# Kernel optimization log

Hardware: AMD Instinct MI355X
Metric: run time of the kernel (lower is better)

## Reference

```python
import jax, jax.numpy as jnp
import numpy as np

N = 100_000   # nodes
E = 1_600_000 # edges (avg degree 16)
B = 512       # graphs in batch
F_IN = 64; H = 4; D = 64; HD = H * D; EXTRA = 16
NEG_SLOPE = 0.2  # DGL GATConv default


def _gat_conv(x, src, dst, W, al, ar, bias):
    """DGL GATConv: fc -> per-head attn logits -> edge leaky_relu -> segment softmax over dst -> scatter-sum."""
    h = (x @ W).reshape(N, H, D)                       # [N,H,D]
    el = jnp.sum(h * al, axis=-1)                      # [N,H]
    er = jnp.sum(h * ar, axis=-1)                      # [N,H]
    e = jax.nn.leaky_relu(el[src] + er[dst], NEG_SLOPE)  # [E,H]
    m = jax.ops.segment_max(e, dst, num_segments=N)    # [N,H]
    m = jnp.where(jnp.isfinite(m), m, 0.0)             # guard empty segments
    ex = jnp.exp(e - m[dst])                           # [E,H]
    den = jax.ops.segment_sum(ex, dst, num_segments=N) # [N,H]
    alpha = ex / jnp.maximum(den[dst], 1e-9)           # [E,H]
    msg = h[src] * alpha[:, :, None]                   # [E,H,D]
    out = jax.ops.segment_sum(msg, dst, num_segments=N) + bias.reshape(1, H, D)
    return out  # [N,H,D]


def setup_inputs() -> dict:
    key = jax.random.key(0)
    ks = jax.random.split(key, 26)
    nrm = lambda k, shape: jax.random.normal(k, shape, dtype=jnp.float32) * 0.5
    src = jax.random.randint(ks[0], (E,), 0, N)
    # ensure every node has >=1 incoming edge (DGL disallows zero in-degree by default)
    dst = jnp.concatenate([jnp.arange(N), jax.random.randint(ks[1], (E - N,), 0, N)])
    node_graph = jnp.sort(jax.random.randint(ks[2], (N,), 0, B))
    inp = dict(
        src=src, dst=dst, node_graph=node_graph,
        feats_node=jax.random.normal(ks[3], (N, F_IN), dtype=jnp.float32),
        feats_graph=jax.random.normal(ks[4], (B, EXTRA), dtype=jnp.float32),
        W1=nrm(ks[5], (F_IN, HD)), al1=nrm(ks[6], (H, D)), ar1=nrm(ks[7], (H, D)), bg1=jnp.zeros(HD),
        W2=nrm(ks[8], (HD, HD)),  al2=nrm(ks[9], (H, D)), ar2=nrm(ks[10], (H, D)), bg2=jnp.zeros(HD),
        W3=nrm(ks[11], (HD, HD)), al3=nrm(ks[12], (H, D)), ar3=nrm(ks[13], (H, D)), bg3=jnp.zeros(HD),
        sw=nrm(ks[14], (HD, 1)), sb=jnp.zeros(1),
        lw1=nrm(ks[15], (HD + EXTRA, 2 * D)), lb1=jnp.zeros(2 * D),
        lw2=nrm(ks[16], (2 * D, D)), lb2=jnp.zeros(D),
        lw3=nrm(ks[17], (D, 1)), lb3=jnp.zeros(1),
    )
    return inp


def reference(src, dst, node_graph, feats_node, feats_graph,
              W1, al1, ar1, bg1, W2, al2, ar2, bg2, W3, al3, ar3, bg3,
              sw, sb, lw1, lb1, lw2, lb2, lw3, lb3):
    selu = jax.nn.selu
    x = selu(_gat_conv(feats_node, src, dst, W1, al1, ar1, bg1)).reshape(N, HD)
    x = selu(_gat_conv(x, src, dst, W2, al2, ar2, bg2)).reshape(N, HD)
    x = selu(_gat_conv(x, src, dst, W3, al3, ar3, bg3)).reshape(N, HD)
    # WeightedAverage readout: sigmoid-scored weighted mean per graph
    w = jax.nn.sigmoid(x @ sw + sb)                               # [N,1]
    num = jax.ops.segment_sum(w * x, node_graph, num_segments=B)  # [B,HD]
    den = jax.ops.segment_sum(w, node_graph, num_segments=B)      # [B,1]
    emb = num / jnp.maximum(den, 1e-9)
    y = jnp.concatenate([emb, feats_graph], axis=1)
    y = selu(y @ lw1 + lb1)
    y = selu(y @ lw2 + lb2)
    return y @ lw3 + lb3  # [B,1]
```

## Files before the change

kernel.cpp:

```cpp
#include <hip/hip_runtime.h>

#define N_NODES 100000
#define N_EDGES 1600000
#define N_GRAPHS 512
#define F_IN 64
#define HD 256
#define EXTRA 16
#define SCAN_BLOCK 512

typedef float f32x4 __attribute__((ext_vector_type(4)));
typedef _Float16 f16x4 __attribute__((ext_vector_type(4)));
typedef _Float16 f16x8 __attribute__((ext_vector_type(8)));

__device__ __forceinline__ float selu_f(float x) {
    const float a = 1.6732632423543772f, sc = 1.0507009873554805f;
    return x > 0.f ? sc * x : sc * a * (__expf(x) - 1.f);
}

__global__ __launch_bounds__(256) void hist_k(const int* __restrict__ dst, int* __restrict__ hist) {
    int j = blockIdx.x * 256 + threadIdx.x;
    if (j < N_EDGES) atomicAdd(&hist[dst[j]], 1);
}

__global__ __launch_bounds__(SCAN_BLOCK) void scan1_k(const int* __restrict__ hist,
                                                      int* __restrict__ row_ptr,
                                                      int* __restrict__ bsums) {
    __shared__ int sm[SCAN_BLOCK];
    int t = threadIdx.x;
    int i = blockIdx.x * SCAN_BLOCK + t;
    int v = (i < N_NODES) ? hist[i] : 0;
    sm[t] = v;
    __syncthreads();
    for (int off = 1; off < SCAN_BLOCK; off <<= 1) {
        int add = (t >= off) ? sm[t - off] : 0;
        __syncthreads();
        sm[t] += add;
        __syncthreads();
    }
    if (i < N_NODES) row_ptr[i] = sm[t] - v;
    if (t == SCAN_BLOCK - 1) bsums[blockIdx.x] = sm[t];
}

__global__ __launch_bounds__(256) void scan2_k(int* __restrict__ bsums, int nb) {
    __shared__ int sm[256];
    int t = threadIdx.x;
    int v = (t < nb) ? bsums[t] : 0;
    sm[t] = v;
    __syncthreads();
    for (int off = 1; off < 256; off <<= 1) {
        int add = (t >= off) ? sm[t - off] : 0;
        __syncthreads();
        sm[t] += add;
        __syncthreads();
    }
    if (t < nb) bsums[t] = sm[t] - v;
}

__global__ __launch_bounds__(256) void scan3_k(int* __restrict__ row_ptr, const int* __restrict__ bsums) {
    int i = blockIdx.x * 256 + threadIdx.x;
    if (i < N_NODES) row_ptr[i] += bsums[i / SCAN_BLOCK];
    if (i == 0) row_ptr[N_NODES] = N_EDGES;
}

__global__ __launch_bounds__(256) void scatter_k(const int* __restrict__ src,
                                                 const int* __restrict__ dst,
                                                 const int* __restrict__ row_ptr,
                                                 int* __restrict__ cursor,
                                                 int* __restrict__ csr_src) {
    int j = blockIdx.x * 256 + threadIdx.x;
    if (j < N_EDGES) {
        int d = dst[j];
        int r = atomicAdd(&cursor[d], 1);
        csr_src[row_ptr[d] + r] = src[j];
    }
}

__global__ __launch_bounds__(256) void gbound_k(const int* __restrict__ node_graph, int* __restrict__ gstart) {
    int g = blockIdx.x * 256 + threadIdx.x;
    if (g > N_GRAPHS) return;
    int lo = 0, hi = N_NODES;
    while (lo < hi) {
        int mid = (lo + hi) >> 1;
        if (node_graph[mid] < g) lo = mid + 1; else hi = mid;
    }
    gstart[g] = lo;
}

__global__ __launch_bounds__(256) void tcast_split_k(const float* __restrict__ W,
                                                     _Float16* __restrict__ Wt_hi,
                                                     _Float16* __restrict__ Wt_lo, int K) {
    int idx = blockIdx.x * 256 + threadIdx.x;
    if (idx >= K * HD) return;
    int n = idx / K, k = idx - n * K;
    float w = W[(size_t)k * HD + n];
    _Float16 hi = (_Float16)w;
    _Float16 lo = (_Float16)(w - (float)hi);
    Wt_hi[idx] = hi;
    Wt_lo[idx] = lo;
}

template <int K>
__global__ __launch_bounds__(256) void gemm_split_k(const float* __restrict__ A,
                                                    const _Float16* __restrict__ Bt_hi,
                                                    const _Float16* __restrict__ Bt_lo,
                                                    const float* __restrict__ al,
                                                    const float* __restrict__ ar,
                                                    _Float16* __restrict__ Chi,
                                                    float* __restrict__ el,
                                                    float* __restrict__ er, int M) {
    const int BM = 128, BN = 128, LDP = 40;
    __shared__ _Float16 As_hi[BM][LDP];
    __shared__ _Float16 As_lo[BM][LDP];
    __shared__ _Float16 Bs_hi[BN][LDP];
    __shared__ _Float16 Bs_lo[BN][LDP];
    int tid = threadIdx.x;
    int wave = tid >> 6, lane = tid & 63;
    int q = lane >> 4, l16 = lane & 15;
    int row0 = blockIdx.y * BM, col0 = blockIdx.x * BN;
    f32x4 acc[2][8] = {};

    for (int k0 = 0; k0 < K; k0 += 32) {
#pragma unroll
        for (int c = 0; c < 4; c++) {
            int cc = tid + c * 256;
            int r = cc >> 3, o = (cc & 7) * 4;
            int gr = row0 + r;
            float4 v = make_float4(0.f, 0.f, 0.f, 0.f);
            if (gr < M) v = *(const float4*)(A + (size_t)gr * K + k0 + o);
            f16x4 hi, lo;
            hi.x = (_Float16)v.x; lo.x = (_Float16)(v.x - (float)hi.x);
            hi.y = (_Float16)v.y; lo.y = (_Float16)(v.y - (float)hi.y);
            hi.z = (_Float16)v.z; lo.z = (_Float16)(v.z - (float)hi.z);
            hi.w = (_Float16)v.w; lo.w = (_Float16)(v.w - (float)hi.w);
            *(f16x4*)&As_hi[r][o] = hi;
            *(f16x4*)&As_lo[r][o] = lo;
        }
#pragma unroll
        for (int c = 0; c < 2; c++) {
            int cc = tid + c * 256;
            int n = cc >> 2, o = (cc & 3) * 8;
            *(f16x8*)&Bs_hi[n][o] = *(const f16x8*)(Bt_hi + (size_t)(col0 + n) * K + k0 + o);
            *(f16x8*)&Bs_lo[n][o] = *(const f16x8*)(Bt_lo + (size_t)(col0 + n) * K + k0 + o);
        }
        __syncthreads();

        f16x8 ah[2], alo2[2];
#pragma unroll
        for (int ms = 0; ms < 2; ms++) {
            int m = wave * 32 + ms * 16 + l16;
            ah[ms] = *(const f16x8*)&As_hi[m][q * 8];
            alo2[ms] = *(const f16x8*)&As_lo[m][q * 8];
        }
#pragma unroll
        for (int ns = 0; ns < 8; ns++) {
            int n = ns * 16 + l16;
            f16x8 bh = *(const f16x8*)&Bs_hi[n][q * 8];
            f16x8 bl = *(const f16x8*)&Bs_lo[n][q * 8];
#pragma unroll
            for (int ms = 0; ms < 2; ms++) {
                acc[ms][ns] = __builtin_amdgcn_mfma_f32_16x16x32_f16(ah[ms], bh, acc[ms][ns], 0, 0, 0);
                acc[ms][ns] = __builtin_amdgcn_mfma_f32_16x16x32_f16(ah[ms], bl, acc[ms][ns], 0, 0, 0);
                acc[ms][ns] = __builtin_amdgcn_mfma_f32_16x16x32_f16(alo2[ms], bh, acc[ms][ns], 0, 0, 0);
            }
        }
        __syncthreads();
    }

    const int h0 = col0 >> 6;
    float alv[8], arv[8];
#pragma unroll
    for (int ns = 0; ns < 8; ns++) {
        int hh = h0 + (ns >> 2);
        int d = (ns & 3) * 16 + l16;
        alv[ns] = al[hh * 64 + d];
        arv[ns] = ar[hh * 64 + d];
    }
#pragma unroll
    for (int ms = 0; ms < 2; ms++) {
#pragma unroll
        for (int i = 0; i < 4; i++) {
            int r = row0 + wave * 32 + ms * 16 + q * 4 + i;
            bool ok = r < M;
            float el0 = 0.f, er0 = 0.f, el1 = 0.f, er1 = 0.f;
#pragma unroll
            for (int ns = 0; ns < 8; ns++) {
                float v = acc[ms][ns][i];
                if (ok) Chi[(size_t)r * HD + col0 + ns * 16 + l16] = (_Float16)v;
                if (ns < 4) { el0 = fmaf(v, alv[ns], el0); er0 = fmaf(v, arv[ns], er0); }
                else        { el1 = fmaf(v, alv[ns], el1); er1 = fmaf(v, arv[ns], er1); }
            }
#pragma unroll
            for (int off = 1; off < 16; off <<= 1) {
                el0 += __shfl_xor(el0, off, 64);
                er0 += __shfl_xor(er0, off, 64);
                el1 += __shfl_xor(el1, off, 64);
                er1 += __shfl_xor(er1, off, 64);
            }
            if (l16 == 0 && ok) {
                el[(size_t)r * 4 + h0] = el0;
                el[(size_t)r * 4 + h0 + 1] = el1;
                er[(size_t)r * 4 + h0] = er0;
                er[(size_t)r * 4 + h0 + 1] = er1;
            }
        }
    }
}

template <int OUT>
__global__ __launch_bounds__(256) void gat_aggregate_k(const _Float16* __restrict__ hb,
                                                       const float* __restrict__ el,
                                                       const float* __restrict__ er,
                                                       const int* __restrict__ csr_src,
                                                       const int* __restrict__ row_ptr,
                                                       const float* __restrict__ bias,
                                                       float* __restrict__ xout,
                                                       const float* __restrict__ sw,
                                                       const float* __restrict__ sb,
                                                       float* __restrict__ wsc) {
    __shared__ float wlds[4][64][4];
    __shared__ int snlds[4][64];
    int wv = threadIdx.x >> 6;
    int lane = threadIdx.x & 63;
    int v = blockIdx.x * 4 + wv;
    bool valid = v < N_NODES;
    int vc = valid ? v : 0;
    int rs = row_ptr[vc];
    int deg = valid ? row_ptr[vc + 1] - rs : 0;
    float4 erv = make_float4(0.f, 0.f, 0.f, 0.f);
    if (valid) erv = *(const float4*)(er + (size_t)vc * 4);

    int head = lane >> 4;
    float inv_den = 1.f;
    float m_h = 0.f, er_h = 0.f;

    if (deg <= 64) {
        float e0 = -1e30f, e1 = -1e30f, e2 = -1e30f, e3 = -1e30f;
        int my_sn = 0;
        if (lane < deg) {
            my_sn = csr_src[rs + lane];
            float4 elv = *(const float4*)(el + (size_t)my_sn * 4);
            float t0 = elv.x + erv.x, t1 = elv.y + erv.y, t2 = elv.z + erv.z, t3 = elv.w + erv.w;
            e0 = t0 > 0.f ? t0 : 0.2f * t0;
            e1 = t1 > 0.f ? t1 : 0.2f * t1;
            e2 = t2 > 0.f ? t2 : 0.2f * t2;
            e3 = t3 > 0.f ? t3 : 0.2f * t3;
        }
        float m0 = e0, m1 = e1, m2 = e2, m3 = e3;
        for (int off = 1; off < deg; off <<= 1) {
            m0 = fmaxf(m0, __shfl_xor(m0, off, 64));
            m1 = fmaxf(m1, __shfl_xor(m1, off, 64));
            m2 = fmaxf(m2, __shfl_xor(m2, off, 64));
            m3 = fmaxf(m3, __shfl_xor(m3, off, 64));
        }
        float p0 = 0.f, p1 = 0.f, p2 = 0.f, p3 = 0.f;
        if (lane < deg) {
            p0 = __expf(e0 - m0); p1 = __expf(e1 - m1);
            p2 = __expf(e2 - m2); p3 = __expf(e3 - m3);
        }
        float s0 = p0, s1 = p1, s2 = p2, s3 = p3;
        for (int off = 1; off < deg; off <<= 1) {
            s0 += __shfl_xor(s0, off, 64);
            s1 += __shfl_xor(s1, off, 64);
            s2 += __shfl_xor(s2, off, 64);
            s3 += __shfl_xor(s3, off, 64);
        }
        float d0 = __shfl(s0, 0, 64), d1 = __shfl(s1, 0, 64);
        float d2 = __shfl(s2, 0, 64), d3 = __shfl(s3, 0, 64);
        float den = head == 0 ? d0 : head == 1 ? d1 : head == 2 ? d2 : d3;
        inv_den = 1.f / fmaxf(den, 1e-9f);
        if (lane < deg) {
            wlds[wv][lane][0] = p0;
            wlds[wv][lane][1] = p1;
            wlds[wv][lane][2] = p2;
            wlds[wv][lane][3] = p3;
            snlds[wv][lane] = my_sn;
        }
    } else {
        float m[4] = {-1e30f, -1e30f, -1e30f, -1e30f};
        float s[4] = {0.f, 0.f, 0.f, 0.f};
        for (int t = lane; t < deg; t += 64) {
            int sn = csr_src[rs + t];
            float4 elv = *(const float4*)(el + (size_t)sn * 4);
            float e[4];
            e[0] = elv.x + erv.x; e[1] = elv.y + erv.y; e[2] = elv.z + erv.z; e[3] = elv.w + erv.w;
#pragma unroll
            for (int hh = 0; hh < 4; hh++) {
                float ev = e[hh] > 0.f ? e[hh] : 0.2f * e[hh];
                float mn = fmaxf(m[hh], ev);
                s[hh] = s[hh] * __expf(m[hh] - mn) + __expf(ev - mn);
                m[hh] = mn;
            }
        }
#pragma unroll
        for (int off = 32; off >= 1; off >>= 1) {
#pragma unroll
            for (int hh = 0; hh < 4; hh++) {
                float mo = __shfl_xor(m[hh], off, 64);
                float so = __shfl_xor(s[hh], off, 64);
                float mn = fmaxf(m[hh], mo);
                s[hh] = s[hh] * __expf(m[hh] - mn) + so * __expf(mo - mn);
                m[hh] = mn;
            }
        }
        m_h = head == 0 ? m[0] : head == 1 ? m[1] : head == 2 ? m[2] : m[3];
        float den = head == 0 ? s[0] : head == 1 ? s[1] : head == 2 ? s[2] : s[3];
        er_h = head == 0 ? erv.x : head == 1 ? erv.y : head == 2 ? erv.z : erv.w;
        inv_den = 1.f / fmaxf(den, 1e-9f);
    }
    __syncthreads();

    float a0 = 0.f, a1 = 0.f, a2 = 0.f, a3 = 0.f;
    if (deg <= 64) {
        int t = 0;
        for (; t + 8 <= deg; t += 8) {
            int sn[8];
            float w[8];
#pragma unroll
            for (int u = 0; u < 8; u++) {
                sn[u] = snlds[wv][t + u];
                w[u] = wlds[wv][t + u][head];
            }
            f16x4 hv[8];
#pragma unroll
            for (int u = 0; u < 8; u++)
                hv[u] = *(const f16x4*)(hb + (size_t)sn[u] * HD + lane * 4);
#pragma unroll
            for (int u = 0; u < 8; u++) {
                a0 = fmaf(w[u], (float)hv[u].x, a0);
                a1 = fmaf(w[u], (float)hv[u].y, a1);
                a2 = fmaf(w[u], (float)hv[u].z, a2);
                a3 = fmaf(w[u], (float)hv[u].w, a3);
            }
        }
        for (; t < deg; t++) {
            int sn = snlds[wv][t];
            float w = wlds[wv][t][head];
            f16x4 hv = *(const f16x4*)(hb + (size_t)sn * HD + lane * 4);
            a0 = fmaf(w, (float)hv.x, a0);
            a1 = fmaf(w, (float)hv.y, a1);
            a2 = fmaf(w, (float)hv.z, a2);
            a3 = fmaf(w, (float)hv.w, a3);
        }
    } else {
        for (int t = 0; t < deg; t++) {
            int sn = csr_src[rs + t];
            float e = el[(size_t)sn * 4 + head] + er_h;
            e = e > 0.f ? e : 0.2f * e;
            float w = __expf(e - m_h);
            f16x4 hv = *(const f16x4*)(hb + (size_t)sn * HD + lane * 4);
            a0 = fmaf(w, (float)hv.x, a0);
            a1 = fmaf(w, (float)hv.y, a1);
            a2 = fmaf(w, (float)hv.z, a2);
            a3 = fmaf(w, (float)hv.w, a3);
        }
    }
    float4 bv = *(const float4*)(bias + lane * 4);
    float4 o;
    o.x = selu_f(fmaf(a0, inv_den, bv.x));
    o.y = selu_f(fmaf(a1, inv_den, bv.y));
    o.z = selu_f(fmaf(a2, inv_den, bv.z));
    o.w = selu_f(fmaf(a3, inv_den, bv.w));
    if (valid) *(float4*)(xout + (size_t)v * HD + lane * 4) = o;

    if constexpr (OUT == 1) {
        float4 sv = *(const float4*)(sw + lane * 4);
        float p = o.x * sv.x + o.y * sv.y + o.z * sv.z + o.w * sv.w;
#pragma unroll
        for (int off = 1; off < 64; off <<= 1) p += __shfl_xor(p, off, 64);
        if (lane == 0 && valid) wsc[v] = 1.f / (1.f + __expf(-(p + sb[0])));
    }
}

__global__ __launch_bounds__(256) void readout_k(const float* __restrict__ x,
                                                 const float* __restrict__ wsc,
                                                 const int* __restrict__ gstart,
                                                 const float* __restrict__ fg,
                                                 float* __restrict__ y0) {
    int g = blockIdx.x;
    int f = threadIdx.x;
    int s = gstart[g], e = gstart[g + 1];
    float num = 0.f, den = 0.f;
#pragma unroll 4
    for (int n = s; n < e; n++) {
        float wn = wsc[n];
        num = fmaf(wn, x[(size_t)n * HD + f], num);
        den += wn;
    }
    float emb = num / fmaxf(den, 1e-9f);
    y0[(size_t)g * 272 + f] = emb;
    if (f < EXTRA) y0[(size_t)g * 272 + 256 + f] = fg[g * EXTRA + f];
}

__global__ __launch_bounds__(128) void mlp_k(const float* __restrict__ y0g,
                                             const float* __restrict__ lw1, const float* __restrict__ lb1,
                                             const float* __restrict__ lw2, const float* __restrict__ lb2,
                                             const float* __restrict__ lw3, const float* __restrict__ lb3,
                                             float* __restrict__ out) {
    __shared__ float y0s[272];
    __shared__ float y1s[128];
    int g = blockIdx.x, t = threadIdx.x;
    for (int i = t; i < 272; i += 128) y0s[i] = y0g[(size_t)g * 272 + i];
    __syncthreads();
    float acc = lb1[t];
    for (int k = 0; k < 272; k++) acc = fmaf(y0s[k], lw1[k * 128 + t], acc);
    y1s[t] = selu_f(acc);
    __syncthreads();
    if (t < 64) {
        float a2 = lb2[t];
        for (int k = 0; k < 128; k++) a2 = fmaf(y1s[k], lw2[k * 64 + t], a2);
        float v2 = selu_f(a2);
        float p = v2 * lw3[t];
#pragma unroll
        for (int off = 1; off < 64; off <<= 1) p += __shfl_xor(p, off, 64);
        if (t == 0) out[g] = p + lb3[0];
    }
}

extern "C" void kernel_launch(void* const* d_in, const int* in_sizes, int n_in,
                              void* d_out, int out_size, void* d_ws, size_t ws_size,
                              hipStream_t stream) {
    const int* src = (const int*)d_in[0];
    const int* dst = (const int*)d_in[1];
    const int* node_graph = (const int*)d_in[2];
    const float* feats_node = (const float*)d_in[3];
    const float* feats_graph = (const float*)d_in[4];
    const float* W1 = (const float*)d_in[5];
    const float* al1 = (const float*)d_in[6];
    const float* ar1 = (const float*)d_in[7];
    const float* bg1 = (const float*)d_in[8];
    const float* W2 = (const float*)d_in[9];
    const float* al2 = (const float*)d_in[10];
    const float* ar2 = (const float*)d_in[11];
    const float* bg2 = (const float*)d_in[12];
    const float* W3 = (const float*)d_in[13];
    const float* al3 = (const float*)d_in[14];
    const float* ar3 = (const float*)d_in[15];
    const float* bg3 = (const float*)d_in[16];
    const float* sw = (const float*)d_in[17];
    const float* sb = (const float*)d_in[18];
    const float* lw1 = (const float*)d_in[19];
    const float* lb1 = (const float*)d_in[20];
    const float* lw2 = (const float*)d_in[21];
    const float* lb2 = (const float*)d_in[22];
    const float* lw3 = (const float*)d_in[23];
    const float* lb3 = (const float*)d_in[24];
    float* out = (float*)d_out;

    char* ws = (char*)d_ws;
    size_t off = 0;
    auto alloc = [&](size_t bytes) -> char* {
        char* p = ws + off;
        off += (bytes + 255) & ~(size_t)255;
        return p;
    };
    float* xf32 = (float*)alloc((size_t)N_NODES * HD * 4);
    _Float16* hhi = (_Float16*)alloc((size_t)N_NODES * HD * 2);
    _Float16* W1hi = (_Float16*)alloc((size_t)F_IN * HD * 2);
    _Float16* W1lo = (_Float16*)alloc((size_t)F_IN * HD * 2);
    _Float16* W2hi = (_Float16*)alloc((size_t)HD * HD * 2);
    _Float16* W2lo = (_Float16*)alloc((size_t)HD * HD * 2);
    _Float16* W3hi = (_Float16*)alloc((size_t)HD * HD * 2);
    _Float16* W3lo = (_Float16*)alloc((size_t)HD * HD * 2);
    float* el = (float*)alloc((size_t)N_NODES * 4 * 4);
    float* er = (float*)alloc((size_t)N_NODES * 4 * 4);
    float* wsc = (float*)alloc((size_t)N_NODES * 4);
    float* y0 = (float*)alloc((size_t)N_GRAPHS * 272 * 4);
    int* hist = (int*)alloc((size_t)N_NODES * 4);
    int* row_ptr = (int*)alloc((size_t)(N_NODES + 1) * 4);
    int* cursor = (int*)alloc((size_t)N_NODES * 4);
    int* csr_src = (int*)alloc((size_t)N_EDGES * 4);
    int* gstart = (int*)alloc((size_t)(N_GRAPHS + 1) * 4);
    int* bsums = (int*)alloc(256 * 4);
    (void)ws_size; (void)in_sizes; (void)n_in; (void)out_size;

    hipMemsetAsync(hist, 0, (size_t)N_NODES * 4, stream);
    hipMemsetAsync(cursor, 0, (size_t)N_NODES * 4, stream);

    hist_k<<<(N_EDGES + 255) / 256, 256, 0, stream>>>(dst, hist);
    int nb = (N_NODES + SCAN_BLOCK - 1) / SCAN_BLOCK;
    scan1_k<<<nb, SCAN_BLOCK, 0, stream>>>(hist, row_ptr, bsums);
    scan2_k<<<1, 256, 0, stream>>>(bsums, nb);
    scan3_k<<<(N_NODES + 255) / 256, 256, 0, stream>>>(row_ptr, bsums);
    scatter_k<<<(N_EDGES + 255) / 256, 256, 0, stream>>>(src, dst, row_ptr, cursor, csr_src);
    gbound_k<<<3, 256, 0, stream>>>(node_graph, gstart);

    tcast_split_k<<<(F_IN * HD + 255) / 256, 256, 0, stream>>>(W1, W1hi, W1lo, F_IN);
    tcast_split_k<<<(HD * HD + 255) / 256, 256, 0, stream>>>(W2, W2hi, W2lo, HD);
    tcast_split_k<<<(HD * HD + 255) / 256, 256, 0, stream>>>(W3, W3hi, W3lo, HD);

    dim3 ggrid(HD / 128, (N_NODES + 127) / 128);
    int nwb = (N_NODES + 3) / 4;

    gemm_split_k<F_IN><<<ggrid, 256, 0, stream>>>(feats_node, W1hi, W1lo, al1, ar1, hhi, el, er, N_NODES);
    gat_aggregate_k<0><<<nwb, 256, 0, stream>>>(hhi, el, er, csr_src, row_ptr, bg1, xf32, nullptr, nullptr, nullptr);
    gemm_split_k<HD><<<ggrid, 256, 0, stream>>>(xf32, W2hi, W2lo, al2, ar2, hhi, el, er, N_NODES);
    gat_aggregate_k<0><<<nwb, 256, 0, stream>>>(hhi, el, er, csr_src, row_ptr, bg2, xf32, nullptr, nullptr, nullptr);
    gemm_split_k<HD><<<ggrid, 256, 0, stream>>>(xf32, W3hi, W3lo, al3, ar3, hhi, el, er, N_NODES);
    gat_aggregate_k<1><<<nwb, 256, 0, stream>>>(hhi, el, er, csr_src, row_ptr, bg3, xf32, sw, sb, wsc);

    readout_k<<<N_GRAPHS, 256, 0, stream>>>(xf32, wsc, gstart, feats_graph, y0);
    mlp_k<<<N_GRAPHS, 128, 0, stream>>>(y0, lw1, lb1, lw2, lb2, lw3, lb3, out);
}
```

Before: 973.0 us.

## Store activations as fp16 hi/lo split, prefetch neighbors, simplify CSR scatter

The aggregate kernel now writes layer outputs directly as fp16 hi/lo pairs, so the following GEMM loads pre-split halves instead of fp32 values and converting in its tile loader. Input features get a separate split-cast kernel. The aggregation prefetches the first eight neighbor rows before the softmax reductions and drops a __syncthreads. The CSR scatter seeds its cursor with row_ptr, which removes a memset and an extra row_ptr read per edge. The split representation moves the same number of bytes as fp32, and the xf32 buffer now aliases xhi.

```diff
diff --git a/kernel.cpp b/kernel.cpp
--- a/kernel.cpp
+++ b/kernel.cpp
@@ -56,22 +56,25 @@
     if (t < nb) bsums[t] = sm[t] - v;
 }
 
-__global__ __launch_bounds__(256) void scan3_k(int* __restrict__ row_ptr, const int* __restrict__ bsums) {
+__global__ __launch_bounds__(256) void scan3_k(int* __restrict__ row_ptr, const int* __restrict__ bsums,
+                                               int* __restrict__ cursor) {
     int i = blockIdx.x * 256 + threadIdx.x;
-    if (i < N_NODES) row_ptr[i] += bsums[i / SCAN_BLOCK];
+    if (i < N_NODES) {
+        int r = row_ptr[i] + bsums[i / SCAN_BLOCK];
+        row_ptr[i] = r;
+        cursor[i] = r;
+    }
     if (i == 0) row_ptr[N_NODES] = N_EDGES;
 }
 
 __global__ __launch_bounds__(256) void scatter_k(const int* __restrict__ src,
                                                  const int* __restrict__ dst,
-                                                 const int* __restrict__ row_ptr,
                                                  int* __restrict__ cursor,
                                                  int* __restrict__ csr_src) {
     int j = blockIdx.x * 256 + threadIdx.x;
     if (j < N_EDGES) {
-        int d = dst[j];
-        int r = atomicAdd(&cursor[d], 1);
-        csr_src[row_ptr[d] + r] = src[j];
+        int r = atomicAdd(&cursor[dst[j]], 1);
+        csr_src[r] = src[j];
     }
 }
 
@@ -99,8 +102,24 @@
     Wt_lo[idx] = lo;
 }
 
+__global__ __launch_bounds__(256) void split_cast_k(const float* __restrict__ in,
+                                                    _Float16* __restrict__ hi,
+                                                    _Float16* __restrict__ lo, int n4) {
+    int i = blockIdx.x * 256 + threadIdx.x;
+    if (i >= n4) return;
+    float4 v = *(const float4*)(in + (size_t)i * 4);
+    f16x4 h, l;
+    h.x = (_Float16)v.x; l.x = (_Float16)(v.x - (float)h.x);
+    h.y = (_Float16)v.y; l.y = (_Float16)(v.y - (float)h.y);
+    h.z = (_Float16)v.z; l.z = (_Float16)(v.z - (float)h.z);
+    h.w = (_Float16)v.w; l.w = (_Float16)(v.w - (float)h.w);
+    *(f16x4*)(hi + (size_t)i * 4) = h;
+    *(f16x4*)(lo + (size_t)i * 4) = l;
+}
+
 template <int K>
-__global__ __launch_bounds__(256) void gemm_split_k(const float* __restrict__ A,
+__global__ __launch_bounds__(256) void gemm_split_k(const _Float16* __restrict__ Ahi,
+                                                    const _Float16* __restrict__ Alo,
                                                     const _Float16* __restrict__ Bt_hi,
                                                     const _Float16* __restrict__ Bt_lo,
                                                     const float* __restrict__ al,
@@ -121,19 +140,17 @@
 
     for (int k0 = 0; k0 < K; k0 += 32) {
 #pragma unroll
-        for (int c = 0; c < 4; c++) {
+        for (int c = 0; c < 2; c++) {
             int cc = tid + c * 256;
-            int r = cc >> 3, o = (cc & 7) * 4;
+            int r = cc >> 2, o = (cc & 3) * 8;
             int gr = row0 + r;
-            float4 v = make_float4(0.f, 0.f, 0.f, 0.f);
-            if (gr < M) v = *(const float4*)(A + (size_t)gr * K + k0 + o);
-            f16x4 hi, lo;
-            hi.x = (_Float16)v.x; lo.x = (_Float16)(v.x - (float)hi.x);
-            hi.y = (_Float16)v.y; lo.y = (_Float16)(v.y - (float)hi.y);
-            hi.z = (_Float16)v.z; lo.z = (_Float16)(v.z - (float)hi.z);
-            hi.w = (_Float16)v.w; lo.w = (_Float16)(v.w - (float)hi.w);
-            *(f16x4*)&As_hi[r][o] = hi;
-            *(f16x4*)&As_lo[r][o] = lo;
+            f16x8 vh = {}, vl = {};
+            if (gr < M) {
+                vh = *(const f16x8*)(Ahi + (size_t)gr * K + k0 + o);
+                vl = *(const f16x8*)(Alo + (size_t)gr * K + k0 + o);
+            }
+            *(f16x8*)&As_hi[r][o] = vh;
+            *(f16x8*)&As_lo[r][o] = vl;
         }
 #pragma unroll
         for (int c = 0; c < 2; c++) {
@@ -213,7 +230,9 @@
                                                        const int* __restrict__ csr_src,
                                                        const int* __restrict__ row_ptr,
                                                        const float* __restrict__ bias,
-                                                       float* __restrict__ xout,
+                                                       _Float16* __restrict__ xhi,
+                                                       _Float16* __restrict__ xlo,
+                                                       float* __restrict__ xf32,
                                                        const float* __restrict__ sw,
                                                        const float* __restrict__ sb,
                                                        float* __restrict__ wsc) {
@@ -232,6 +251,8 @@
     int head = lane >> 4;
     float inv_den = 1.f;
     float m_h = 0.f, er_h = 0.f;
+    f16x4 hv_pre[8];
+    int nb0 = 0;
 
     if (deg <= 64) {
         float e0 = -1e30f, e1 = -1e30f, e2 = -1e30f, e3 = -1e30f;
@@ -245,6 +266,12 @@
             e2 = t2 > 0.f ? t2 : 0.2f * t2;
             e3 = t3 > 0.f ? t3 : 0.2f * t3;
         }
+        nb0 = deg < 8 ? deg : 8;
+#pragma unroll
+        for (int u = 0; u < 8; u++) {
+            int snb = __shfl(my_sn, u, 64);
+            if (u < nb0) hv_pre[u] = *(const f16x4*)(hb + (size_t)snb * HD + lane * 4);
+        }
         float m0 = e0, m1 = e1, m2 = e2, m3 = e3;
         for (int off = 1; off < deg; off <<= 1) {
             m0 = fmaxf(m0, __shfl_xor(m0, off, 64));
@@ -307,11 +334,20 @@
         er_h = head == 0 ? erv.x : head == 1 ? erv.y : head == 2 ? erv.z : erv.w;
         inv_den = 1.f / fmaxf(den, 1e-9f);
     }
-    __syncthreads();
 
     float a0 = 0.f, a1 = 0.f, a2 = 0.f, a3 = 0.f;
     if (deg <= 64) {
-        int t = 0;
+#pragma unroll
+        for (int u = 0; u < 8; u++) {
+            if (u < nb0) {
+                float w = wlds[wv][u][head];
+                a0 = fmaf(w, (float)hv_pre[u].x, a0);
+                a1 = fmaf(w, (float)hv_pre[u].y, a1);
+                a2 = fmaf(w, (float)hv_pre[u].z, a2);
+                a3 = fmaf(w, (float)hv_pre[u].w, a3);
+            }
+        }
+        int t = 8;
         for (; t + 8 <= deg; t += 8) {
             int sn[8];
             float w[8];
@@ -360,9 +396,19 @@
     o.y = selu_f(fmaf(a1, inv_den, bv.y));
     o.z = selu_f(fmaf(a2, inv_den, bv.z));
     o.w = selu_f(fmaf(a3, inv_den, bv.w));
-    if (valid) *(float4*)(xout + (size_t)v * HD + lane * 4) = o;
-
-    if constexpr (OUT == 1) {
+
+    if constexpr (OUT == 0) {
+        f16x4 oh, ol;
+        oh.x = (_Float16)o.x; ol.x = (_Float16)(o.x - (float)oh.x);
+        oh.y = (_Float16)o.y; ol.y = (_Float16)(o.y - (float)oh.y);
+        oh.z = (_Float16)o.z; ol.z = (_Float16)(o.z - (float)oh.z);
+        oh.w = (_Float16)o.w; ol.w = (_Float16)(o.w - (float)oh.w);
+        if (valid) {
+            *(f16x4*)(xhi + (size_t)v * HD + lane * 4) = oh;
+            *(f16x4*)(xlo + (size_t)v * HD + lane * 4) = ol;
+        }
+    } else {
+        if (valid) *(float4*)(xf32 + (size_t)v * HD + lane * 4) = o;
         float4 sv = *(const float4*)(sw + lane * 4);
         float p = o.x * sv.x + o.y * sv.y + o.z * sv.z + o.w * sv.w;
 #pragma unroll
@@ -453,8 +499,12 @@
         off += (bytes + 255) & ~(size_t)255;
         return p;
     };
-    float* xf32 = (float*)alloc((size_t)N_NODES * HD * 4);
+    _Float16* xhi = (_Float16*)alloc((size_t)N_NODES * HD * 2);
+    _Float16* xlo = (_Float16*)alloc((size_t)N_NODES * HD * 2);
+    float* xf32 = (float*)xhi;
     _Float16* hhi = (_Float16*)alloc((size_t)N_NODES * HD * 2);
+    _Float16* fhi = (_Float16*)alloc((size_t)N_NODES * F_IN * 2);
+    _Float16* flo = (_Float16*)alloc((size_t)N_NODES * F_IN * 2);
     _Float16* W1hi = (_Float16*)alloc((size_t)F_IN * HD * 2);
     _Float16* W1lo = (_Float16*)alloc((size_t)F_IN * HD * 2);
     _Float16* W2hi = (_Float16*)alloc((size_t)HD * HD * 2);
@@ -474,16 +524,16 @@
     (void)ws_size; (void)in_sizes; (void)n_in; (void)out_size;
 
     hipMemsetAsync(hist, 0, (size_t)N_NODES * 4, stream);
-    hipMemsetAsync(cursor, 0, (size_t)N_NODES * 4, stream);
 
     hist_k<<<(N_EDGES + 255) / 256, 256, 0, stream>>>(dst, hist);
     int nb = (N_NODES + SCAN_BLOCK - 1) / SCAN_BLOCK;
     scan1_k<<<nb, SCAN_BLOCK, 0, stream>>>(hist, row_ptr, bsums);
     scan2_k<<<1, 256, 0, stream>>>(bsums, nb);
-    scan3_k<<<(N_NODES + 255) / 256, 256, 0, stream>>>(row_ptr, bsums);
-    scatter_k<<<(N_EDGES + 255) / 256, 256, 0, stream>>>(src, dst, row_ptr, cursor, csr_src);
+    scan3_k<<<(N_NODES + 255) / 256, 256, 0, stream>>>(row_ptr, bsums, cursor);
+    scatter_k<<<(N_EDGES + 255) / 256, 256, 0, stream>>>(src, dst, cursor, csr_src);
     gbound_k<<<3, 256, 0, stream>>>(node_graph, gstart);
 
+    split_cast_k<<<(N_NODES * F_IN / 4 + 255) / 256, 256, 0, stream>>>(feats_node, fhi, flo, N_NODES * F_IN / 4);
     tcast_split_k<<<(F_IN * HD + 255) / 256, 256, 0, stream>>>(W1, W1hi, W1lo, F_IN);
     tcast_split_k<<<(HD * HD + 255) / 256, 256, 0, stream>>>(W2, W2hi, W2lo, HD);
     tcast_split_k<<<(HD * HD + 255) / 256, 256, 0, stream>>>(W3, W3hi, W3lo, HD);
@@ -491,12 +541,12 @@
     dim3 ggrid(HD / 128, (N_NODES + 127) / 128);
     int nwb = (N_NODES + 3) / 4;
 
-    gemm_split_k<F_IN><<<ggrid, 256, 0, stream>>>(feats_node, W1hi, W1lo, al1, ar1, hhi, el, er, N_NODES);
-    gat_aggregate_k<0><<<nwb, 256, 0, stream>>>(hhi, el, er, csr_src, row_ptr, bg1, xf32, nullptr, nullptr, nullptr);
-    gemm_split_k<HD><<<ggrid, 256, 0, stream>>>(xf32, W2hi, W2lo, al2, ar2, hhi, el, er, N_NODES);
-    gat_aggregate_k<0><<<nwb, 256, 0, stream>>>(hhi, el, er, csr_src, row_ptr, bg2, xf32, nullptr, nullptr, nullptr);
-    gemm_split_k<HD><<<ggrid, 256, 0, stream>>>(xf32, W3hi, W3lo, al3, ar3, hhi, el, er, N_NODES);
-    gat_aggregate_k<1><<<nwb, 256, 0, stream>>>(hhi, el, er, csr_src, row_ptr, bg3, xf32, sw, sb, wsc);
+    gemm_split_k<F_IN><<<ggrid, 256, 0, stream>>>(fhi, flo, W1hi, W1lo, al1, ar1, hhi, el, er, N_NODES);
+    gat_aggregate_k<0><<<nwb, 256, 0, stream>>>(hhi, el, er, csr_src, row_ptr, bg1, xhi, xlo, nullptr, nullptr, nullptr, nullptr);
+    gemm_split_k<HD><<<ggrid, 256, 0, stream>>>(xhi, xlo, W2hi, W2lo, al2, ar2, hhi, el, er, N_NODES);
+    gat_aggregate_k<0><<<nwb, 256, 0, stream>>>(hhi, el, er, csr_src, row_ptr, bg2, xhi, xlo, nullptr, nullptr, nullptr, nullptr);
+    gemm_split_k<HD><<<ggrid, 256, 0, stream>>>(xhi, xlo, W3hi, W3lo, al3, ar3, hhi, el, er, N_NODES);
+    gat_aggregate_k<1><<<nwb, 256, 0, stream>>>(hhi, el, er, csr_src, row_ptr, bg3, nullptr, nullptr, xf32, sw, sb, wsc);
 
     readout_k<<<N_GRAPHS, 256, 0, stream>>>(xf32, wsc, gstart, feats_graph, y0);
     mlp_k<<<N_GRAPHS, 128, 0, stream>>>(y0, lw1, lb1, lw2, lb2, lw3, lb3, out);
```

Result: faster. 952.8 us (-2.1%).
